# Performance work log

Hardware: AMD Instinct MI355X
Metric: run time of the kernel (lower is better)

## Reference

```python
import jax, jax.numpy as jnp
import numpy as np

N_EMBD = 1024  # C in forward; scale is C**-0.5 (full embed dim, per source)


def setup_inputs() -> dict:
    key = jax.random.key(0)
    k1, k2, k3, k4 = jax.random.split(key, 4)
    B, T, C, H = 4, 4096, N_EMBD, 64
    x = jax.random.normal(k1, (B, T, C), dtype=jnp.float32)
    # weights stored as [in, out] = [n_embd, head_size]
    Wq = jax.random.normal(k2, (C, H), dtype=jnp.float32) * (C ** -0.5)
    Wk = jax.random.normal(k3, (C, H), dtype=jnp.float32) * (C ** -0.5)
    Wv = jax.random.normal(k4, (C, H), dtype=jnp.float32) * (C ** -0.5)
    return {"x": x, "Wq": Wq, "Wk": Wk, "Wv": Wv}


def reference(x, Wq, Wk, Wv):
    # x: [B, T, C]; projections to head_size H
    C = x.shape[-1]
    q = jnp.einsum('btc,ch->bth', x, Wq)  # [B,T,H]
    k = jnp.einsum('btc,ch->bth', x, Wk)  # [B,T,H]
    v = jnp.einsum('btc,ch->bth', x, Wv)  # [B,T,H]
    # scores scaled by C**-0.5 (full embed dim, matching original module)
    wei = jnp.einsum('bth,bsh->bts', q, k) * (C ** -0.5)  # [B,T,T]
    wei = jax.nn.softmax(wei, axis=-1)  # dropout p=0 -> identity
    out = jnp.einsum('bts,bsh->bth', wei, v)  # [B,T,H]
    return out
```

## Files before the change

kernel.cpp:

```cpp
#include <hip/hip_runtime.h>
#include <hip/hip_bf16.h>


#define BB 4
#define TT 4096
#define CC 1024
#define HH 64

typedef __attribute__((ext_vector_type(8))) short bf16x8;
typedef __attribute__((ext_vector_type(4))) float f32x4;

#if __has_builtin(__builtin_amdgcn_exp2f)
#define EXP2(x) __builtin_amdgcn_exp2f(x)
#else
#define EXP2(x) exp2f(x)
#endif

__device__ __forceinline__ short f2bf(float f) {
  union { float f; unsigned u; } v; v.f = f;
  unsigned r = v.u + 0x7fffu + ((v.u >> 16) & 1u);
  return (short)(r >> 16);
}

__device__ __forceinline__ short p2bf(float f) {
  union { float f; unsigned u; } v; v.f = f;
  return (short)((v.u + 0x8000u) >> 16);
}

__global__ void wtf_kernel(const float* __restrict__ Wq, const float* __restrict__ Wk,
                           const float* __restrict__ Wv, short* __restrict__ WtF) {
  int idx = blockIdx.x * 256 + threadIdx.x;
  int lane = idx & 63, ks = (idx >> 6) & 31, nf = idx >> 11;
  int l15 = lane & 15, lg = lane >> 4;
  int n = nf * 16 + l15;
  const float* W = (n < HH) ? Wq : ((n < 2 * HH) ? Wk : Wv);
  float sc = (n < HH) ? (0.03125f * 1.44269504f) : 1.0f;
  int k0 = ks * 32 + lg * 8, h = n & (HH - 1);
  bf16x8 r;
#pragma unroll
  for (int j = 0; j < 8; ++j) r[j] = f2bf(W[(k0 + j) * HH + h] * sc);
  *(bf16x8*)(WtF + (size_t)idx * 8) = r;
}

__launch_bounds__(256, 4)
__global__ void proj_kernel(const float* __restrict__ x, const short* __restrict__ WtF,
                            short* __restrict__ qo, short* __restrict__ ko,
                            short* __restrict__ vTo) {
  __shared__ __align__(16) short xs[16 * 1024];
  int t = threadIdx.x;
  int row0 = blockIdx.x * 16;

  {
    int r = t >> 4, kc = t & 15;
    const float4* xr4 = (const float4*)(x + (size_t)(row0 + r) * CC) + kc * 2;
#pragma unroll
    for (int i = 0; i < 8; ++i) {
      float4 a = xr4[i * 32], b2 = xr4[i * 32 + 1];
      bf16x8 w;
      w[0] = f2bf(a.x);  w[1] = f2bf(a.y);  w[2] = f2bf(a.z);  w[3] = f2bf(a.w);
      w[4] = f2bf(b2.x); w[5] = f2bf(b2.y); w[6] = f2bf(b2.z); w[7] = f2bf(b2.w);
      int c = kc + i * 16;
      int S = (c * 256 + r * 16) ^ ((c & 7) << 4);
      *(bf16x8*)((char*)xs + S) = w;
    }
  }
  __syncthreads();

  int wave = t >> 6, lane = t & 63;
  int l15 = lane & 15, lg = lane >> 4;
  int nf0 = wave * 3;
  const short* wp = WtF + ((size_t)nf0 * 32 * 64 + (size_t)lane) * 8;
  const char* xsb = (const char*)xs;

  f32x4 acc[3];
#pragma unroll
  for (int j = 0; j < 3; ++j) acc[j] = (f32x4){0.f, 0.f, 0.f, 0.f};

  bf16x8 wA[3], wB[3];
#pragma unroll
  for (int j = 0; j < 3; ++j) wA[j] = *(const bf16x8*)(wp + (size_t)j * 32 * 512);

#pragma unroll
  for (int ks = 0; ks < 32; ks += 2) {
#pragma unroll
    for (int j = 0; j < 3; ++j)
      wB[j] = *(const bf16x8*)(wp + ((size_t)j * 32 + ks + 1) * 512);
    bf16x8 a0 = *(const bf16x8*)(xsb + ks * 1024 +
                   ((lane * 16) ^ ((((ks * 4) + lg) & 7) << 4)));
#pragma unroll
    for (int j = 0; j < 3; ++j)
      acc[j] = __builtin_amdgcn_mfma_f32_16x16x32_bf16(a0, wA[j], acc[j], 0, 0, 0);
    if (ks + 2 < 32) {
#pragma unroll
      for (int j = 0; j < 3; ++j)
        wA[j] = *(const bf16x8*)(wp + ((size_t)j * 32 + ks + 2) * 512);
    }
    bf16x8 a1 = *(const bf16x8*)(xsb + (ks + 1) * 1024 +
                   ((lane * 16) ^ (((((ks + 1) * 4) + lg) & 7) << 4)));
#pragma unroll
    for (int j = 0; j < 3; ++j)
      acc[j] = __builtin_amdgcn_mfma_f32_16x16x32_bf16(a1, wB[j], acc[j], 0, 0, 0);
  }

#pragma unroll
  for (int j = 0; j < 3; ++j) {
    int nf = nf0 + j;
    int h = (nf & 3) * 16 + l15;
    if (nf < 8) {
      short* dst = (nf < 4) ? qo : ko;
#pragma unroll
      for (int reg = 0; reg < 4; ++reg)
        dst[(size_t)(row0 + lg * 4 + reg) * HH + h] = f2bf(acc[j][reg]);
    } else {
      int b = row0 >> 12;
      int trow = (row0 & 4095) + lg * 4;
      short4 s4;
      s4.x = f2bf(acc[j][0]); s4.y = f2bf(acc[j][1]);
      s4.z = f2bf(acc[j][2]); s4.w = f2bf(acc[j][3]);
      *(short4*)(vTo + ((size_t)b * HH + h) * TT + trow) = s4;
    }
  }
}

__global__ void kperm_kernel(const short* __restrict__ k, short* __restrict__ kF) {
  int idx = blockIdx.x * 256 + threadIdx.x;
  int lane = idx & 63, ld = (idx >> 6) & 7, kt = (idx >> 9) & 63, b = idx >> 15;
  int l15 = lane & 15, lg = lane >> 4;
  int kpos = kt * 64 + (ld >> 1) * 16 + l15;
  int e0 = (ld & 1) * 32 + lg * 8;
  bf16x8 r = *(const bf16x8*)(k + ((size_t)b * TT + kpos) * HH + e0);
  *(bf16x8*)(kF + (size_t)idx * 8) = r;
}

__global__ void vperm_kernel(const short* __restrict__ vT, short* __restrict__ vF) {
  int idx = blockIdx.x * 256 + threadIdx.x;
  int lane = idx & 63, ld = (idx >> 6) & 7, kt = (idx >> 9) & 63, b = idx >> 15;
  int l15 = lane & 15, lg = lane >> 4;
  int h = (ld >> 1) * 16 + l15;
  int spos = kt * 64 + (ld & 1) * 32 + lg * 8;
  bf16x8 r = *(const bf16x8*)(vT + ((size_t)b * HH + h) * TT + spos);
  *(bf16x8*)(vF + (size_t)idx * 8) = r;
}

__launch_bounds__(512, 4)
__global__ void attnW_kernel(const short* __restrict__ q, const short* __restrict__ kF,
                             const short* __restrict__ vF, float* __restrict__ out) {
  __shared__ __align__(16) short ps[8][2560];
  __shared__ __align__(16) float macc[32][68];
  __shared__ float lL[32];
  int wave = threadIdx.x >> 6, lane = threadIdx.x & 63;
  int l15 = lane & 15, lg = lane >> 4;
  int low3 = blockIdx.x & 7;
  int b  = low3 >> 1;
  int qt = ((blockIdx.x >> 3) << 1) | (low3 & 1);
  int brow0 = qt * 32;

  const short* qb = q + ((size_t)b * TT + brow0 + l15) * HH;
  bf16x8 qa[2][2];
#pragma unroll
  for (int g = 0; g < 2; ++g) {
    qa[g][0] = *(const bf16x8*)(qb + g * 16 * HH + lg * 8);
    qa[g][1] = *(const bf16x8*)(qb + g * 16 * HH + 32 + lg * 8);
  }

  bf16x8 ones;
#pragma unroll
  for (int j = 0; j < 8; ++j) ones[j] = (short)0x3F80;

  const short* kfb = kF + (size_t)b * 262144 + (size_t)lane * 8;
  const short* vfb = vF + (size_t)b * 262144 + (size_t)lane * 8;

  f32x4 acc[2][4], accl[2];
#pragma unroll
  for (int g = 0; g < 2; ++g) {
#pragma unroll
    for (int i = 0; i < 4; ++i) acc[g][i] = (f32x4){0.f, 0.f, 0.f, 0.f};
    accl[g] = (f32x4){0.f, 0.f, 0.f, 0.f};
  }

  char* psw = (char*)&ps[wave][0];
  int pw = lg * 320 + ((l15 * 2) ^ ((lg >> 1) << 4));
  int pr = l15 * 80 + ((lg ^ (l15 >> 3)) << 4);

  for (int t = wave * 16; t < wave * 16 + 16; ++t) {
    const short* kp = kfb + (size_t)t * 2048;
    const short* vp = vfb + (size_t)(t >> 1) * 4096 + (size_t)(t & 1) * 512;
    bf16x8 kf[4], vf[4];
#pragma unroll
    for (int ld = 0; ld < 4; ++ld) kf[ld] = *(const bf16x8*)(kp + ld * 512);
#pragma unroll
    for (int hf = 0; hf < 4; ++hf) vf[hf] = *(const bf16x8*)(vp + hf * 1024);
#pragma unroll
    for (int g = 0; g < 2; ++g)
#pragma unroll
      for (int cf = 0; cf < 2; ++cf) {
        f32x4 t4 = (f32x4){0.f, 0.f, 0.f, 0.f};
        t4 = __builtin_amdgcn_mfma_f32_16x16x32_bf16(qa[g][0], kf[cf * 2], t4, 0, 0, 0);
        t4 = __builtin_amdgcn_mfma_f32_16x16x32_bf16(qa[g][1], kf[cf * 2 + 1], t4, 0, 0, 0);
#pragma unroll
        for (int reg = 0; reg < 4; ++reg) {
          float p = EXP2(t4[reg]);
          *(short*)(psw + (g * 1280 + pw + reg * 80 + cf * 32)) = p2bf(p);
        }
      }
    bf16x8 pa0 = *(const bf16x8*)(psw + pr);
    bf16x8 pa1 = *(const bf16x8*)(psw + 1280 + pr);
    __builtin_amdgcn_s_setprio(1);
#pragma unroll
    for (int hf = 0; hf < 4; ++hf) {
      acc[0][hf] = __builtin_amdgcn_mfma_f32_16x16x32_bf16(pa0, vf[hf], acc[0][hf], 0, 0, 0);
      acc[1][hf] = __builtin_amdgcn_mfma_f32_16x16x32_bf16(pa1, vf[hf], acc[1][hf], 0, 0, 0);
    }
    accl[0] = __builtin_amdgcn_mfma_f32_16x16x32_bf16(pa0, ones, accl[0], 0, 0, 0);
    accl[1] = __builtin_amdgcn_mfma_f32_16x16x32_bf16(pa1, ones, accl[1], 0, 0, 0);
    __builtin_amdgcn_s_setprio(0);
  }

#pragma unroll
  for (int ph = 0; ph < 8; ++ph) {
    if (wave == ph) {
#pragma unroll
      for (int g = 0; g < 2; ++g)
#pragma unroll
        for (int reg = 0; reg < 4; ++reg) {
          int row = g * 16 + lg * 4 + reg;
          if (ph == 0) {
#pragma unroll
            for (int hf = 0; hf < 4; ++hf)
              macc[row][hf * 16 + l15] = acc[g][hf][reg];
            if (l15 == 0) lL[row] = accl[g][reg];
          } else {
#pragma unroll
            for (int hf = 0; hf < 4; ++hf)
              macc[row][hf * 16 + l15] += acc[g][hf][reg];
            if (l15 == 0) lL[row] += accl[g][reg];
          }
        }
    }
    __syncthreads();
  }

  {
    int tt = threadIdx.x;
    int r = tt >> 4, c0 = (tt & 15) * 4;
    float linv = 1.0f / lL[r];
    float4 o;
    o.x = macc[r][c0 + 0] * linv; o.y = macc[r][c0 + 1] * linv;
    o.z = macc[r][c0 + 2] * linv; o.w = macc[r][c0 + 3] * linv;
    *(float4*)(out + ((size_t)b * TT + brow0 + r) * HH + c0) = o;
  }
}

extern "C" void kernel_launch(void* const* d_in, const int* in_sizes, int n_in,
                              void* d_out, int out_size, void* d_ws, size_t ws_size,
                              hipStream_t stream) {
  const float* x  = (const float*)d_in[0];
  const float* Wq = (const float*)d_in[1];
  const float* Wk = (const float*)d_in[2];
  const float* Wv = (const float*)d_in[3];
  float* out = (float*)d_out;

  char* ws = (char*)d_ws;
  short* WtF = (short*)ws;
  short* q   = (short*)(ws + 0x080000);
  short* k   = (short*)(ws + 0x280000);
  short* vT  = (short*)(ws + 0x480000);
  short* kF  = (short*)(ws + 0x680000);
  short* vF  = (short*)(ws + 0x880000);

  hipLaunchKernelGGL(wtf_kernel,   dim3(96),   dim3(256), 0, stream, Wq, Wk, Wv, WtF);
  hipLaunchKernelGGL(proj_kernel,  dim3(1024), dim3(256), 0, stream, x, WtF, q, k, vT);
  hipLaunchKernelGGL(kperm_kernel, dim3(512),  dim3(256), 0, stream, k, kF);
  hipLaunchKernelGGL(vperm_kernel, dim3(512),  dim3(256), 0, stream, vT, vF);
  hipLaunchKernelGGL(attnW_kernel, dim3(512),  dim3(512), 0, stream, q, kF, vF, out);
}
```

Before: 69.29 us.

## Fuse K/V fragment permutation into projection kernel epilogue via shared memory

The projection kernel now stages its K and V results in shared memory, reusing the x tile buffer after a barrier, and writes them straight out in the MFMA fragment layout the attention kernel consumes. This removes the two separate permutation kernels, their launches, and the global round-trip through the intermediate k and vT buffers. It adds two block-wide barriers and some LDS traffic to the projection epilogue.

```diff
diff --git a/kernel.cpp b/kernel.cpp
--- a/kernel.cpp
+++ b/kernel.cpp
@@ -44,8 +44,8 @@
 
 __launch_bounds__(256, 4)
 __global__ void proj_kernel(const float* __restrict__ x, const short* __restrict__ WtF,
-                            short* __restrict__ qo, short* __restrict__ ko,
-                            short* __restrict__ vTo) {
+                            short* __restrict__ qo, short* __restrict__ kFo,
+                            short* __restrict__ vFo) {
   __shared__ __align__(16) short xs[16 * 1024];
   int t = threadIdx.x;
   int row0 = blockIdx.x * 16;
@@ -102,44 +102,48 @@
       acc[j] = __builtin_amdgcn_mfma_f32_16x16x32_bf16(a1, wB[j], acc[j], 0, 0, 0);
   }
 
+  int b  = row0 >> 12;
+  int kt = (row0 & 4095) >> 6;
+  int cf = (row0 >> 4) & 3;
+  short* ksl = xs;
+  short* vsl = xs + 1152;
+
+  __syncthreads();
+
 #pragma unroll
   for (int j = 0; j < 3; ++j) {
     int nf = nf0 + j;
     int h = (nf & 3) * 16 + l15;
-    if (nf < 8) {
-      short* dst = (nf < 4) ? qo : ko;
+    if (nf < 4) {
 #pragma unroll
       for (int reg = 0; reg < 4; ++reg)
-        dst[(size_t)(row0 + lg * 4 + reg) * HH + h] = f2bf(acc[j][reg]);
+        qo[(size_t)(row0 + lg * 4 + reg) * HH + h] = f2bf(acc[j][reg]);
+    } else if (nf < 8) {
+#pragma unroll
+      for (int reg = 0; reg < 4; ++reg)
+        ksl[(lg * 4 + reg) * 72 + h] = f2bf(acc[j][reg]);
     } else {
-      int b = row0 >> 12;
-      int trow = (row0 & 4095) + lg * 4;
       short4 s4;
       s4.x = f2bf(acc[j][0]); s4.y = f2bf(acc[j][1]);
       s4.z = f2bf(acc[j][2]); s4.w = f2bf(acc[j][3]);
-      *(short4*)(vTo + ((size_t)b * HH + h) * TT + trow) = s4;
-    }
-  }
-}
-
-__global__ void kperm_kernel(const short* __restrict__ k, short* __restrict__ kF) {
-  int idx = blockIdx.x * 256 + threadIdx.x;
-  int lane = idx & 63, ld = (idx >> 6) & 7, kt = (idx >> 9) & 63, b = idx >> 15;
-  int l15 = lane & 15, lg = lane >> 4;
-  int kpos = kt * 64 + (ld >> 1) * 16 + l15;
-  int e0 = (ld & 1) * 32 + lg * 8;
-  bf16x8 r = *(const bf16x8*)(k + ((size_t)b * TT + kpos) * HH + e0);
-  *(bf16x8*)(kF + (size_t)idx * 8) = r;
-}
-
-__global__ void vperm_kernel(const short* __restrict__ vT, short* __restrict__ vF) {
-  int idx = blockIdx.x * 256 + threadIdx.x;
-  int lane = idx & 63, ld = (idx >> 6) & 7, kt = (idx >> 9) & 63, b = idx >> 15;
-  int l15 = lane & 15, lg = lane >> 4;
-  int h = (ld >> 1) * 16 + l15;
-  int spos = kt * 64 + (ld & 1) * 32 + lg * 8;
-  bf16x8 r = *(const bf16x8*)(vT + ((size_t)b * HH + h) * TT + spos);
-  *(bf16x8*)(vF + (size_t)idx * 8) = r;
+      *(short4*)(vsl + h * 24 + lg * 4) = s4;
+    }
+  }
+  __syncthreads();
+
+  size_t tileoff = ((size_t)b * 64 + kt) * 4096;
+  if (t < 128) {
+    int ks2 = t >> 6, ln = t & 63;
+    int l15o = ln & 15, lgo = ln >> 4;
+    bf16x8 r = *(const bf16x8*)(ksl + l15o * 72 + ks2 * 32 + lgo * 8);
+    *(bf16x8*)(kFo + tileoff + (size_t)(cf * 2 + ks2) * 512 + ln * 8) = r;
+  } else if (t < 256) {
+    int t2 = t - 128;
+    int hf = t2 >> 5, lgl = (t2 >> 4) & 1, l15o = t2 & 15;
+    bf16x8 r = *(const bf16x8*)(vsl + (hf * 16 + l15o) * 24 + lgl * 8);
+    int lnout = (2 * (cf & 1) + lgl) * 16 + l15o;
+    *(bf16x8*)(vFo + tileoff + (size_t)(hf * 2 + (cf >> 1)) * 512 + lnout * 8) = r;
+  }
 }
 
 __launch_bounds__(512, 4)
@@ -263,14 +267,10 @@
   char* ws = (char*)d_ws;
   short* WtF = (short*)ws;
   short* q   = (short*)(ws + 0x080000);
-  short* k   = (short*)(ws + 0x280000);
-  short* vT  = (short*)(ws + 0x480000);
-  short* kF  = (short*)(ws + 0x680000);
-  short* vF  = (short*)(ws + 0x880000);
+  short* kF  = (short*)(ws + 0x280000);
+  short* vF  = (short*)(ws + 0x480000);
 
   hipLaunchKernelGGL(wtf_kernel,   dim3(96),   dim3(256), 0, stream, Wq, Wk, Wv, WtF);
-  hipLaunchKernelGGL(proj_kernel,  dim3(1024), dim3(256), 0, stream, x, WtF, q, k, vT);
-  hipLaunchKernelGGL(kperm_kernel, dim3(512),  dim3(256), 0, stream, k, kF);
-  hipLaunchKernelGGL(vperm_kernel, dim3(512),  dim3(256), 0, stream, vT, vF);
+  hipLaunchKernelGGL(proj_kernel,  dim3(1024), dim3(256), 0, stream, x, WtF, q, kF, vF);
   hipLaunchKernelGGL(attnW_kernel, dim3(512),  dim3(512), 0, stream, q, kF, vF, out);
 }
```

After: 64.42 us. 7.0% less time.
